# Kernel optimization log

Hardware: AMD Instinct MI355X
Metric: run time of the kernel (lower is better)

The kernel has to match this reference:

```python
import jax, jax.numpy as jnp
import numpy as np

N, E, B, D, L = 100000, 600000, 128, 128, 3
BOT = 64
EPS = 1e-5


def _forward(query_x, corpus_x, gin_eps, mlp_W1, mlp_b1, mlp_W2, mlp_b2, bn_gamma, bn_beta,
             pool_G1, pool_g1b, pool_G2, pool_g2b, pool_Wm,
             int_G1, int_g1b, int_G2, int_g2b, int_F1, int_f1b, int_F2, int_f2b,
             sc_G1, sc_g1b, sc_G2, sc_g2b, sc_F1, sc_f1b, sc_F2, sc_f2b,
             query_edge_index, query_graph_idx, corpus_edge_index, corpus_graph_idx, num_graphs):
    def gin(x, ei, l):
        # GINConv: sum of source-node features into targets, plus (1+eps)*self
        agg = jax.ops.segment_sum(x[ei[0]], ei[1], num_segments=x.shape[0])
        h = (1.0 + gin_eps[l]) * x + agg
        h = jax.nn.relu(h @ mlp_W1[l] + mlp_b1[l]) @ mlp_W2[l] + mlp_b2[l]
        mu = h.mean(axis=0)
        var = ((h - mu) ** 2).mean(axis=0)  # biased var (BatchNorm training mode)
        h = (h - mu) * jax.lax.rsqrt(var + EPS) * bn_gamma[l] + bn_beta[l]
        return jax.nn.relu(h)  # dropout p=0.0

    def pool(x, gidx, l):
        coef = jnp.tanh(jax.nn.relu(x @ pool_G1[l] + pool_g1b[l]) @ pool_G2[l] + pool_g2b[l])
        s = (coef + 1.0) * x
        sums = jax.ops.segment_sum(s, gidx, num_segments=num_graphs)
        cnt = jax.ops.segment_sum(jnp.ones((x.shape[0],), x.dtype), gidx, num_segments=num_graphs)
        mean = sums / cnt[:, None]
        gc = jnp.tanh(mean @ pool_Wm[l])  # [B, D]
        node_coef = jax.nn.sigmoid(jnp.sum(s * gc[gidx], axis=1))  # [N]
        return jax.ops.segment_sum(node_coef[:, None] * s, gidx, num_segments=num_graphs)

    def interact(q, c, l):
        comb = jnp.concatenate([q, c], axis=1)  # [B, 2D]
        coef = jax.nn.sigmoid(jax.nn.relu(comb @ int_G1[l] + int_g1b[l]) @ int_G2[l] + int_g2b[l])
        sc = (coef + 1.0) * comb
        return jax.nn.relu(jax.nn.relu(sc @ int_F1[l] + int_f1b[l]) @ int_F2[l] + int_f2b[l])

    qx, cx = query_x, corpus_x
    feats = []
    for l in range(gin_eps.shape[0]):
        qx = gin(qx, query_edge_index, l)
        cx = gin(cx, corpus_edge_index, l)
        feats.append(interact(pool(qx, query_graph_idx, l), pool(cx, corpus_graph_idx, l), l))
    f = jnp.concatenate(feats, axis=1)  # [B, sum(filters)//2]
    coef = jax.nn.sigmoid(jax.nn.relu(f @ sc_G1 + sc_g1b) @ sc_G2 + sc_g2b)
    sf = (coef + 1.0) * f
    return (jax.nn.relu(sf @ sc_F1 + sc_f1b) @ sc_F2 + sc_f2b).squeeze(-1)  # [B]


def setup_inputs() -> dict:
    key = jax.random.key(0)
    kit = iter(jax.random.split(key, 64))
    def nrm(shape, s=0.05):
        return jax.random.normal(next(kit), shape, jnp.float32) * s
    C, R, OUT, AGG, RG = 2 * D, (2 * D) // 4, D // 2, (3 * D) // 2, ((3 * D) // 2) // 4
    inp = {
        "query_x": nrm((N, D), 1.0),
        "query_edge_index": jax.random.randint(next(kit), (2, E), 0, N),
        "query_graph_idx": jnp.sort(jax.random.randint(next(kit), (N,), 0, B)),
        "corpus_x": nrm((N, D), 1.0),
        "corpus_edge_index": jax.random.randint(next(kit), (2, E), 0, N),
        "corpus_graph_idx": jnp.sort(jax.random.randint(next(kit), (N,), 0, B)),
        "num_graphs": B,
        "gin_eps": jnp.zeros((L,), jnp.float32),
        "mlp_W1": nrm((L, D, D)), "mlp_b1": jnp.zeros((L, D)),
        "mlp_W2": nrm((L, D, D)), "mlp_b2": jnp.zeros((L, D)),
        "bn_gamma": jnp.ones((L, D)), "bn_beta": jnp.zeros((L, D)),
        "pool_G1": nrm((L, D, D // 4)), "pool_g1b": jnp.zeros((L, D // 4)),
        "pool_G2": nrm((L, D // 4, D)), "pool_g2b": jnp.zeros((L, D)),
        "pool_Wm": nrm((L, D, D)),
        "int_G1": nrm((L, C, R)), "int_g1b": jnp.zeros((L, R)),
        "int_G2": nrm((L, R, C)), "int_g2b": jnp.zeros((L, C)),
        "int_F1": nrm((L, C, C)), "int_f1b": jnp.zeros((L, C)),
        "int_F2": nrm((L, C, OUT)), "int_f2b": jnp.zeros((L, OUT)),
        "sc_G1": nrm((AGG, RG)), "sc_g1b": jnp.zeros((RG,)),
        "sc_G2": nrm((RG, AGG)), "sc_g2b": jnp.zeros((AGG,)),
        "sc_F1": nrm((AGG, BOT)), "sc_f1b": jnp.zeros((BOT,)),
        "sc_F2": nrm((BOT, 1)), "sc_f2b": jnp.zeros((1,)),
    }
    return inp


def reference(query_x, query_edge_index, query_graph_idx, corpus_x, corpus_edge_index, corpus_graph_idx,
              num_graphs, gin_eps, mlp_W1, mlp_b1, mlp_W2, mlp_b2, bn_gamma, bn_beta,
              pool_G1, pool_g1b, pool_G2, pool_g2b, pool_Wm,
              int_G1, int_g1b, int_G2, int_g2b, int_F1, int_f1b, int_F2, int_f2b,
              sc_G1, sc_g1b, sc_G2, sc_g2b, sc_F1, sc_f1b, sc_F2, sc_f2b):
    return _forward(query_x, corpus_x, gin_eps, mlp_W1, mlp_b1, mlp_W2, mlp_b2, bn_gamma, bn_beta,
                    pool_G1, pool_g1b, pool_G2, pool_g2b, pool_Wm,
                    int_G1, int_g1b, int_G2, int_g2b, int_F1, int_f1b, int_F2, int_f2b,
                    sc_G1, sc_g1b, sc_G2, sc_g2b, sc_F1, sc_f1b, sc_F2, sc_f2b,
                    query_edge_index, query_graph_idx, corpus_edge_index, corpus_graph_idx, num_graphs)
```

## Files before the change

kernel.cpp:

```cpp
#include <hip/hip_runtime.h>
#include <hip/hip_bf16.h>

constexpr int NN  = 100000;
constexpr int NN2 = 200000;
constexpr int NE  = 600000;
constexpr int NB  = 128;
constexpr int D   = 128;
constexpr int NL  = 3;
constexpr int CAP = 48;
constexpr int MT_TOT = NN2 / 16;
constexpr int MT_Q   = NN / 16;

typedef __bf16 bf16x8 __attribute__((ext_vector_type(8)));
typedef float f32x4 __attribute__((ext_vector_type(4)));
typedef unsigned short us8 __attribute__((ext_vector_type(8)));

__device__ __forceinline__ float sigmoidf_(float x) { return 1.0f / (1.0f + __expf(-x)); }
__device__ __forceinline__ unsigned short f2b(float f) {
    __hip_bfloat16 h = __float2bfloat16(f);
    return __builtin_bit_cast(unsigned short, h);
}
__device__ __forceinline__ float b2f(unsigned short u) {
    __hip_bfloat16 h = __builtin_bit_cast(__hip_bfloat16, u);
    return __bfloat162float(h);
}
__device__ __forceinline__ bf16x8 ldfrag(const unsigned short* p) {
    return __builtin_bit_cast(bf16x8, *(const us8*)p);
}

__global__ __launch_bounds__(256) void k_csr_fill(const int* __restrict__ qei, const int* __restrict__ cei,
                                                  int* __restrict__ deg, int* __restrict__ bucket) {
    int e = blockIdx.x * 256 + threadIdx.x;
    int src, dst;
    if (e < NE) {
        src = qei[e]; dst = qei[NE + e];
    } else if (e < 2 * NE) {
        src = cei[e - NE] + NN; dst = cei[NE + (e - NE)] + NN;
    } else return;
    int pos = atomicAdd(&deg[dst], 1);
    if (pos < CAP) bucket[(size_t)dst * CAP + pos] = src;
}

__global__ __launch_bounds__(256) void k_cnt(const int* __restrict__ gq, const int* __restrict__ gc,
                                             float* __restrict__ cnt) {
    __shared__ float h[256];
    for (int i = threadIdx.x; i < 256; i += 256) h[i] = 0.f;
    __syncthreads();
    int total = gridDim.x * 256;
    int tid = blockIdx.x * 256 + threadIdx.x;
    int per = (NN2 + total - 1) / total;
    int r0 = tid * per, r1 = min(r0 + per, NN2);
    if (r0 < r1) {
        int cur = (r0 < NN) ? gq[r0] : 128 + gc[r0 - NN];
        float c = 0.f;
        for (int r = r0; r < r1; ++r) {
            int g = (r < NN) ? gq[r] : 128 + gc[r - NN];
            if (g != cur) { atomicAdd(&h[cur], c); c = 0.f; cur = g; }
            c += 1.f;
        }
        atomicAdd(&h[cur], c);
    }
    __syncthreads();
    for (int i = threadIdx.x; i < 256; i += 256)
        if (h[i] != 0.f) atomicAdd(&cnt[i], h[i]);
}

__global__ __launch_bounds__(256) void k_wprep_all(
    const float* mW1, const float* mW2, const float* pG1, const float* pG2,
    const float* iG1, const float* iG2, const float* iF1, const float* iF2,
    const float* sG1, const float* sG2, const float* sF1,
    unsigned short* W1t, unsigned short* W2t, unsigned short* G1t, unsigned short* G2t,
    unsigned short* iG1t, unsigned short* iG2t, unsigned short* iF1t, unsigned short* iF2t,
    unsigned short* sG1t, unsigned short* sG2t, unsigned short* sF1t) {
    int i = blockIdx.x * 256 + threadIdx.x;
#define SEG(CNT, KK, NN_, SRC, DST)                                              \
    if (i < (CNT)) {                                                             \
        int l = i / ((KK) * (NN_)), r = i % ((KK) * (NN_));                      \
        int n = r / (KK), k = r % (KK);                                          \
        DST[i] = f2b(SRC[(size_t)l * (KK) * (NN_) + (size_t)k * (NN_) + n]);     \
        return;                                                                  \
    }                                                                            \
    i -= (CNT);
    SEG(49152, 128, 128, mW1, W1t)
    SEG(49152, 128, 128, mW2, W2t)
    SEG(12288, 128, 32, pG1, G1t)
    SEG(12288, 32, 128, pG2, G2t)
    SEG(49152, 256, 64, iG1, iG1t)
    SEG(49152, 64, 256, iG2, iG2t)
    SEG(196608, 256, 256, iF1, iF1t)
    SEG(49152, 256, 64, iF2, iF2t)
    SEG(9216, 192, 48, sG1, sG1t)
    if (i < 12288) {
        int n = i / 64, k = i % 64;
        sG2t[i] = (k < 48) ? f2b(sG2[(size_t)k * 192 + n]) : (unsigned short)0;
        return;
    }
    i -= 12288;
    SEG(12288, 192, 64, sF1, sF1t)
#undef SEG
}

template <bool BF16IN>
__global__ __launch_bounds__(256) void k_gather(const float* __restrict__ qx, const float* __restrict__ cx,
                                                const unsigned short* __restrict__ xb, unsigned short* __restrict__ z,
                                                const int* __restrict__ deg, const int* __restrict__ bucket,
                                                const float* __restrict__ eps_p, int l) {
    int r = blockIdx.x * 16 + (threadIdx.x >> 4);
    int c8 = threadIdx.x & 15;
    float e = 1.0f + eps_p[l];
    float a[8];
    const float* base = nullptr; int off = 0;
    if constexpr (BF16IN) {
        us8 v = *(const us8*)(xb + (size_t)r * D + c8 * 8);
#pragma unroll
        for (int j = 0; j < 8; ++j) a[j] = e * b2f(v[j]);
    } else {
        base = (r < NN) ? qx : cx; off = (r < NN) ? 0 : NN;
        float4 v0 = *(const float4*)(base + (size_t)(r - off) * D + c8 * 8);
        float4 v1 = *(const float4*)(base + (size_t)(r - off) * D + c8 * 8 + 4);
        a[0] = e * v0.x; a[1] = e * v0.y; a[2] = e * v0.z; a[3] = e * v0.w;
        a[4] = e * v1.x; a[5] = e * v1.y; a[6] = e * v1.z; a[7] = e * v1.w;
    }
    int d = deg[r]; d = (d < CAP) ? d : CAP;
    const int* bk = bucket + (size_t)r * CAP;
    int i = 0;
    for (; i + 4 <= d; i += 4) {
        int s0 = bk[i], s1 = bk[i + 1], s2 = bk[i + 2], s3 = bk[i + 3];
        if constexpr (BF16IN) {
            us8 u0 = *(const us8*)(xb + (size_t)s0 * D + c8 * 8);
            us8 u1 = *(const us8*)(xb + (size_t)s1 * D + c8 * 8);
            us8 u2 = *(const us8*)(xb + (size_t)s2 * D + c8 * 8);
            us8 u3 = *(const us8*)(xb + (size_t)s3 * D + c8 * 8);
#pragma unroll
            for (int j = 0; j < 8; ++j)
                a[j] += b2f(u0[j]) + b2f(u1[j]) + b2f(u2[j]) + b2f(u3[j]);
        } else {
            const float* p0 = base + (size_t)(s0 - off) * D + c8 * 8;
            const float* p1 = base + (size_t)(s1 - off) * D + c8 * 8;
            const float* p2 = base + (size_t)(s2 - off) * D + c8 * 8;
            const float* p3 = base + (size_t)(s3 - off) * D + c8 * 8;
            float4 w0 = *(const float4*)p0, w0b = *(const float4*)(p0 + 4);
            float4 w1 = *(const float4*)p1, w1b = *(const float4*)(p1 + 4);
            float4 w2 = *(const float4*)p2, w2b = *(const float4*)(p2 + 4);
            float4 w3 = *(const float4*)p3, w3b = *(const float4*)(p3 + 4);
            a[0] += w0.x + w1.x + w2.x + w3.x; a[1] += w0.y + w1.y + w2.y + w3.y;
            a[2] += w0.z + w1.z + w2.z + w3.z; a[3] += w0.w + w1.w + w2.w + w3.w;
            a[4] += w0b.x + w1b.x + w2b.x + w3b.x; a[5] += w0b.y + w1b.y + w2b.y + w3b.y;
            a[6] += w0b.z + w1b.z + w2b.z + w3b.z; a[7] += w0b.w + w1b.w + w2b.w + w3b.w;
        }
    }
    for (; i < d; ++i) {
        int s0 = bk[i];
        if constexpr (BF16IN) {
            us8 u0 = *(const us8*)(xb + (size_t)s0 * D + c8 * 8);
#pragma unroll
            for (int j = 0; j < 8; ++j) a[j] += b2f(u0[j]);
        } else {
            const float* p0 = base + (size_t)(s0 - off) * D + c8 * 8;
            float4 w0 = *(const float4*)p0, w0b = *(const float4*)(p0 + 4);
            a[0] += w0.x; a[1] += w0.y; a[2] += w0.z; a[3] += w0.w;
            a[4] += w0b.x; a[5] += w0b.y; a[6] += w0b.z; a[7] += w0b.w;
        }
    }
    us8 o;
#pragma unroll
    for (int j = 0; j < 8; ++j) o[j] = f2b(a[j]);
    *(us8*)(z + (size_t)r * D + c8 * 8) = o;
}

constexpr int HSTR = 136;
__global__ __launch_bounds__(256, 2) void k_mlp(unsigned short* zh,
                                                const unsigned short* __restrict__ W1t,
                                                const unsigned short* __restrict__ W2t,
                                                const float* __restrict__ b1,
                                                const float* __restrict__ b2,
                                                float* __restrict__ stat) {
    __shared__ unsigned short hb[2][2][16 * HSTR];
    __shared__ float red[512];
    int wave = threadIdx.x >> 6, lane = threadIdx.x & 63;
    int col16 = lane & 15, quad = lane >> 4;
    int g = wave >> 1, half = wave & 1;
    bf16x8 bf1[4][4], bf2[4][4];
    float bb1[4], bb2[4];
#pragma unroll
    for (int t = 0; t < 4; ++t) {
        int c = half * 64 + t * 16 + col16;
        bb1[t] = b1[c]; bb2[t] = b2[c];
#pragma unroll
        for (int kc = 0; kc < 4; ++kc) {
            bf1[t][kc] = ldfrag(W1t + (size_t)c * D + kc * 32 + quad * 8);
            bf2[t][kc] = ldfrag(W2t + (size_t)c * D + kc * 32 + quad * 8);
        }
    }
    float cs[2][4] = {{0.f,0.f,0.f,0.f},{0.f,0.f,0.f,0.f}};
    float cq[2][4] = {{0.f,0.f,0.f,0.f},{0.f,0.f,0.f,0.f}};
    int groups = gridDim.x * 2;
    int iters = (MT_TOT + groups - 1) / groups;
    for (int n = 0; n < iters; ++n) {
        int mt = blockIdx.x * 2 + g + n * groups;
        bool act = (mt < MT_TOT);
        int pp = n & 1;
        unsigned short* hbuf = hb[pp][g];
        {
            const unsigned short* Ap = zh + ((size_t)(act ? mt : 0) * 16 + col16) * D + quad * 8;
            f32x4 acc[4];
#pragma unroll
            for (int t = 0; t < 4; ++t) acc[t] = (f32x4){0.f, 0.f, 0.f, 0.f};
#pragma unroll
            for (int kc = 0; kc < 4; ++kc) {
                bf16x8 af = ldfrag(Ap + kc * 32);
#pragma unroll
                for (int t = 0; t < 4; ++t)
                    acc[t] = __builtin_amdgcn_mfma_f32_16x16x32_bf16(af, bf1[t][kc], acc[t], 0, 0, 0);
            }
#pragma unroll
            for (int t = 0; t < 4; ++t) {
                int c = half * 64 + t * 16 + col16;
#pragma unroll
                for (int r = 0; r < 4; ++r)
                    hbuf[(quad * 4 + r) * HSTR + c] = f2b(fmaxf(acc[t][r] + bb1[t], 0.f));
            }
        }
        __syncthreads();
        {
            f32x4 acc[4];
#pragma unroll
            for (int t = 0; t < 4; ++t) acc[t] = (f32x4){0.f, 0.f, 0.f, 0.f};
#pragma unroll
            for (int kc = 0; kc < 4; ++kc) {
                bf16x8 af = ldfrag(&hbuf[col16 * HSTR + kc * 32 + quad * 8]);
#pragma unroll
                for (int t = 0; t < 4; ++t)
                    acc[t] = __builtin_amdgcn_mfma_f32_16x16x32_bf16(af, bf2[t][kc], acc[t], 0, 0, 0);
            }
            if (act) {
                int side = (mt < MT_Q) ? 0 : 1;
#pragma unroll
                for (int t = 0; t < 4; ++t) {
                    int c = half * 64 + t * 16 + col16;
#pragma unroll
                    for (int r = 0; r < 4; ++r) {
                        int m = mt * 16 + quad * 4 + r;
                        float v = acc[t][r] + bb2[t];
                        zh[(size_t)m * D + c] = f2b(v);
                        cs[side][t] += v; cq[side][t] += v * v;
                    }
                }
            }
        }
    }
    for (int i = threadIdx.x; i < 512; i += 256) red[i] = 0.f;
    __syncthreads();
#pragma unroll
    for (int t = 0; t < 4; ++t) {
        int c = half * 64 + t * 16 + col16;
#pragma unroll
        for (int side = 0; side < 2; ++side) {
            atomicAdd(&red[side * 256 + c], cs[side][t]);
            atomicAdd(&red[side * 256 + 128 + c], cq[side][t]);
        }
    }
    __syncthreads();
    for (int i = threadIdx.x; i < 512; i += 256) atomicAdd(&stat[i], red[i]);
}

__global__ __launch_bounds__(256, 2) void k_pool(const unsigned short* __restrict__ H,
                                                 const unsigned short* __restrict__ G1t,
                                                 const unsigned short* __restrict__ G2t,
                                                 const float* __restrict__ b1,
                                                 const float* __restrict__ b2,
                                                 const float* __restrict__ stat,
                                                 const float* __restrict__ gamma,
                                                 const float* __restrict__ beta,
                                                 const int* __restrict__ gq, const int* __restrict__ gcix,
                                                 unsigned short* __restrict__ Xo,
                                                 unsigned short* __restrict__ S,
                                                 float* __restrict__ seg_sum) {
    __shared__ float sc_s[256], sh_s[256];
    __shared__ unsigned short xt[4][16 * HSTR];
    __shared__ unsigned short t2t[4][16 * 40];
    {
        int t = threadIdx.x, side = t >> 7, c = t & 127;
        const float invN = 1.0f / (float)NN;
        float mu = stat[side * 256 + c] * invN;
        float var = fmaxf(stat[side * 256 + 128 + c] * invN - mu * mu, 0.f);
        float inv = rsqrtf(var + 1e-5f);
        float s = gamma[c] * inv;
        sc_s[t] = s;
        sh_s[t] = beta[c] - mu * s;
    }
    __syncthreads();
    int wave = threadIdx.x >> 6, lane = threadIdx.x & 63;
    int col16 = lane & 15, quad = lane >> 4;
    unsigned short* xtile = xt[wave];
    unsigned short* t2tile = t2t[wave];
    int nwaves = gridDim.x * 4;
    int per = (MT_TOT + nwaves - 1) / nwaves;
    int wid = blockIdx.x * 4 + wave;
    int mt0 = wid * per, mt1 = min(mt0 + per, MT_TOT);
    if (mt0 >= mt1) return;

    bf16x8 g1f[2][4], g2f[8];
    float bb1[2], bb2[8];
#pragma unroll
    for (int t = 0; t < 2; ++t) {
        int c = t * 16 + col16;
        bb1[t] = b1[c];
#pragma unroll
        for (int kc = 0; kc < 4; ++kc)
            g1f[t][kc] = ldfrag(G1t + (size_t)c * D + kc * 32 + quad * 8);
    }
#pragma unroll
    for (int t = 0; t < 8; ++t) {
        int c = t * 16 + col16;
        bb2[t] = b2[c];
        g2f[t] = ldfrag(G2t + (size_t)c * 32 + quad * 8);
    }
    float sacc[8] = {0.f, 0.f, 0.f, 0.f, 0.f, 0.f, 0.f, 0.f};
    int curg = -1;
    for (int mt = mt0; mt < mt1; ++mt) {
        int side = (mt < MT_Q) ? 0 : 1;
        const float* scp = sc_s + side * 128;
        const float* shp = sh_s + side * 128;
        const unsigned short* Hp = H + ((size_t)mt * 16 + col16) * D + quad * 8;
        unsigned short* Xp = Xo + ((size_t)mt * 16 + col16) * D + quad * 8;
        f32x4 acc1[2];
#pragma unroll
        for (int t = 0; t < 2; ++t) acc1[t] = (f32x4){0.f, 0.f, 0.f, 0.f};
#pragma unroll
        for (int kc = 0; kc < 4; ++kc) {
            us8 hv = *(const us8*)(Hp + kc * 32);
            int k0 = kc * 32 + quad * 8;
            float4 s0 = *(const float4*)&scp[k0], s1 = *(const float4*)&scp[k0 + 4];
            float4 h0 = *(const float4*)&shp[k0], h1 = *(const float4*)&shp[k0 + 4];
            us8 xv;
            xv[0] = f2b(fmaxf(b2f(hv[0]) * s0.x + h0.x, 0.f));
            xv[1] = f2b(fmaxf(b2f(hv[1]) * s0.y + h0.y, 0.f));
            xv[2] = f2b(fmaxf(b2f(hv[2]) * s0.z + h0.z, 0.f));
            xv[3] = f2b(fmaxf(b2f(hv[3]) * s0.w + h0.w, 0.f));
            xv[4] = f2b(fmaxf(b2f(hv[4]) * s1.x + h1.x, 0.f));
            xv[5] = f2b(fmaxf(b2f(hv[5]) * s1.y + h1.y, 0.f));
            xv[6] = f2b(fmaxf(b2f(hv[6]) * s1.z + h1.z, 0.f));
            xv[7] = f2b(fmaxf(b2f(hv[7]) * s1.w + h1.w, 0.f));
            *(us8*)(Xp + kc * 32) = xv;
            *(us8*)(xtile + col16 * HSTR + k0) = xv;
            bf16x8 af = __builtin_bit_cast(bf16x8, xv);
#pragma unroll
            for (int t = 0; t < 2; ++t)
                acc1[t] = __builtin_amdgcn_mfma_f32_16x16x32_bf16(af, g1f[t][kc], acc1[t], 0, 0, 0);
        }
#pragma unroll
        for (int t = 0; t < 2; ++t) {
            int c = t * 16 + col16;
#pragma unroll
            for (int r = 0; r < 4; ++r)
                t2tile[(quad * 4 + r) * 40 + c] = f2b(fmaxf(acc1[t][r] + bb1[t], 0.f));
        }
        bf16x8 af2 = ldfrag(t2tile + col16 * 40 + quad * 8);
        f32x4 acc2[8];
#pragma unroll
        for (int t = 0; t < 8; ++t) {
            acc2[t] = (f32x4){0.f, 0.f, 0.f, 0.f};
            acc2[t] = __builtin_amdgcn_mfma_f32_16x16x32_bf16(af2, g2f[t], acc2[t], 0, 0, 0);
        }
#pragma unroll
        for (int r = 0; r < 4; ++r) {
            int m = mt * 16 + quad * 4 + r;
            int g = (m < NN) ? gq[m] : 128 + gcix[m - NN];
            if (g != curg) {
                if (curg >= 0) {
#pragma unroll
                    for (int t = 0; t < 8; ++t) {
                        atomicAdd(&seg_sum[(size_t)curg * D + t * 16 + col16], sacc[t]);
                        sacc[t] = 0.f;
                    }
                }
                curg = g;
            }
#pragma unroll
            for (int t = 0; t < 8; ++t) {
                int c = t * 16 + col16;
                float v = (tanhf(acc2[t][r] + bb2[t]) + 1.f) * b2f(xtile[(quad * 4 + r) * HSTR + c]);
                S[(size_t)m * D + c] = f2b(v);
                sacc[t] += v;
            }
        }
    }
    if (curg >= 0) {
#pragma unroll
        for (int t = 0; t < 8; ++t)
            atomicAdd(&seg_sum[(size_t)curg * D + t * 16 + col16], sacc[t]);
    }
}

__global__ void k_gc(const float* __restrict__ sums, const float* __restrict__ cnt,
                     const float* __restrict__ Wm, float* __restrict__ gc) {
    __shared__ float m[D];
    int b = blockIdx.x, j = threadIdx.x;
    m[j] = sums[b * D + j] / cnt[b];
    __syncthreads();
    float a = 0.f;
#pragma unroll 8
    for (int i = 0; i < D; ++i) a += m[i] * Wm[i * D + j];
    gc[b * D + j] = tanhf(a);
}

__global__ __launch_bounds__(256) void k_ncseg(const unsigned short* __restrict__ S,
                                               const int* __restrict__ gq, const int* __restrict__ gc,
                                               const float* __restrict__ gcb,
                                               float* __restrict__ dq, float* __restrict__ dc) {
    int stream = blockIdx.x * 4 + (threadIdx.x >> 6);
    int lane = threadIdx.x & 63;
    int nstream = gridDim.x * 4;
    int per = (NN2 + nstream - 1) / nstream;
    int r0 = stream * per;
    int r1 = min(r0 + per, NN2);
    if (r0 >= r1) return;
    float a0 = 0.f, a1 = 0.f;
    int cur = (r0 < NN) ? gq[r0] : 128 + gc[r0 - NN];
    for (int r = r0; r < r1; ++r) {
        int g = (r < NN) ? gq[r] : 128 + gc[r - NN];
        if (g != cur) {
            float* base = (cur < 128) ? (dq + cur * D) : (dc + (cur - 128) * D);
            atomicAdd(&base[lane * 2], a0);
            atomicAdd(&base[lane * 2 + 1], a1);
            a0 = 0.f; a1 = 0.f; cur = g;
        }
        ushort2 sv = *(const ushort2*)&S[(size_t)r * D + lane * 2];
        float2 gv = *(const float2*)&gcb[(size_t)g * D + lane * 2];
        float v0 = b2f(sv.x), v1 = b2f(sv.y);
        float p = v0 * gv.x + v1 * gv.y;
#pragma unroll
        for (int off = 1; off < 64; off <<= 1) p += __shfl_xor(p, off, 64);
        float nc = sigmoidf_(p);
        a0 += nc * v0; a1 += nc * v1;
    }
    float* base = (cur < 128) ? (dq + cur * D) : (dc + (cur - 128) * D);
    atomicAdd(&base[lane * 2], a0);
    atomicAdd(&base[lane * 2 + 1], a1);
}

constexpr int LSTR = 264;
__global__ __launch_bounds__(256) void k_interact(const float* __restrict__ pooled,
                                                  const unsigned short* __restrict__ iG1t, const float* __restrict__ ig1b,
                                                  const unsigned short* __restrict__ iG2t, const float* __restrict__ ig2b,
                                                  const unsigned short* __restrict__ iF1t, const float* __restrict__ if1b,
                                                  const unsigned short* __restrict__ iF2t, const float* __restrict__ if2b,
                                                  unsigned short* __restrict__ featsb) {
    __shared__ unsigned short bufC[16 * LSTR];
    __shared__ unsigned short bufA[16 * LSTR];
    __shared__ unsigned short bufB[16 * LSTR];
    int t = threadIdx.x, wave = t >> 6, lane = t & 63;
    int col16 = lane & 15, quad = lane >> 4;
    int pg = blockIdx.x & 7, l = blockIdx.x >> 3;
    int p0 = pg * 16;
    {
        int r = t >> 4, c0 = (t & 15) * 16;
        const float* src = (c0 < 128)
            ? (pooled + (size_t)l * NB * D + (size_t)(p0 + r) * D + c0)
            : (pooled + (size_t)(NL + l) * NB * D + (size_t)(p0 + r) * D + (c0 - 128));
#pragma unroll
        for (int j = 0; j < 16; ++j) bufC[r * LSTR + c0 + j] = f2b(src[j]);
    }
    __syncthreads();
    {
        f32x4 acc = (f32x4){0.f, 0.f, 0.f, 0.f};
        int n = wave * 16 + col16;
#pragma unroll
        for (int kc = 0; kc < 8; ++kc) {
            bf16x8 af = ldfrag(&bufC[col16 * LSTR + kc * 32 + quad * 8]);
            bf16x8 bfr = ldfrag(iG1t + ((size_t)l * 64 + n) * 256 + kc * 32 + quad * 8);
            acc = __builtin_amdgcn_mfma_f32_16x16x32_bf16(af, bfr, acc, 0, 0, 0);
        }
        float bb = ig1b[(size_t)l * 64 + n];
#pragma unroll
        for (int r = 0; r < 4; ++r)
            bufA[(quad * 4 + r) * LSTR + n] = f2b(fmaxf(acc[r] + bb, 0.f));
    }
    __syncthreads();
    {
        f32x4 acc[4];
#pragma unroll
        for (int tt = 0; tt < 4; ++tt) acc[tt] = (f32x4){0.f, 0.f, 0.f, 0.f};
#pragma unroll
        for (int kc = 0; kc < 2; ++kc) {
            bf16x8 af = ldfrag(&bufA[col16 * LSTR + kc * 32 + quad * 8]);
#pragma unroll
            for (int tt = 0; tt < 4; ++tt) {
                int n = wave * 64 + tt * 16 + col16;
                bf16x8 bfr = ldfrag(iG2t + ((size_t)l * 256 + n) * 64 + kc * 32 + quad * 8);
                acc[tt] = __builtin_amdgcn_mfma_f32_16x16x32_bf16(af, bfr, acc[tt], 0, 0, 0);
            }
        }
#pragma unroll
        for (int tt = 0; tt < 4; ++tt) {
            int n = wave * 64 + tt * 16 + col16;
            float bb = ig2b[(size_t)l * 256 + n];
#pragma unroll
            for (int r = 0; r < 4; ++r) {
                int row = quad * 4 + r;
                float s = (sigmoidf_(acc[tt][r] + bb) + 1.f) * b2f(bufC[row * LSTR + n]);
                bufB[row * LSTR + n] = f2b(s);
            }
        }
    }
    __syncthreads();
    {
        f32x4 acc[4];
#pragma unroll
        for (int tt = 0; tt < 4; ++tt) acc[tt] = (f32x4){0.f, 0.f, 0.f, 0.f};
#pragma unroll
        for (int kc = 0; kc < 8; ++kc) {
            bf16x8 af = ldfrag(&bufB[col16 * LSTR + kc * 32 + quad * 8]);
#pragma unroll
            for (int tt = 0; tt < 4; ++tt) {
                int n = wave * 64 + tt * 16 + col16;
                bf16x8 bfr = ldfrag(iF1t + (size_t)l * 256 * 256 + (size_t)n * 256 + kc * 32 + quad * 8);
                acc[tt] = __builtin_amdgcn_mfma_f32_16x16x32_bf16(af, bfr, acc[tt], 0, 0, 0);
            }
        }
#pragma unroll
        for (int tt = 0; tt < 4; ++tt) {
            int n = wave * 64 + tt * 16 + col16;
            float bb = if1b[(size_t)l * 256 + n];
#pragma unroll
            for (int r = 0; r < 4; ++r)
                bufA[(quad * 4 + r) * LSTR + n] = f2b(fmaxf(acc[tt][r] + bb, 0.f));
        }
    }
    __syncthreads();
    {
        f32x4 acc = (f32x4){0.f, 0.f, 0.f, 0.f};
        int n = wave * 16 + col16;
#pragma unroll
        for (int kc = 0; kc < 8; ++kc) {
            bf16x8 af = ldfrag(&bufA[col16 * LSTR + kc * 32 + quad * 8]);
            bf16x8 bfr = ldfrag(iF2t + ((size_t)l * 64 + n) * 256 + kc * 32 + quad * 8);
            acc = __builtin_amdgcn_mfma_f32_16x16x32_bf16(af, bfr, acc, 0, 0, 0);
        }
        float bb = if2b[(size_t)l * 64 + n];
#pragma unroll
        for (int r = 0; r < 4; ++r)
            featsb[(size_t)(p0 + quad * 4 + r) * 192 + l * 64 + n] = f2b(fmaxf(acc[r] + bb, 0.f));
    }
}

__global__ __launch_bounds__(256) void k_score(const unsigned short* __restrict__ featsb,
                                               const unsigned short* __restrict__ sG1t, const float* __restrict__ sg1b,
                                               const unsigned short* __restrict__ sG2t, const float* __restrict__ sg2b,
                                               const unsigned short* __restrict__ sF1t, const float* __restrict__ sf1b,
                                               const float* __restrict__ sF2, const float* __restrict__ sf2b,
                                               float* __restrict__ out) {
    __shared__ unsigned short bufF[16 * 200];
    __shared__ unsigned short bufA[16 * LSTR];
    __shared__ unsigned short bufB[16 * LSTR];
    __shared__ float redf[16 * 65];
    int t = threadIdx.x, wave = t >> 6, lane = t & 63;
    int col16 = lane & 15, quad = lane >> 4;
    int p0 = blockIdx.x * 16;
    {
        int r = t >> 4, c0 = (t & 15) * 12;
#pragma unroll
        for (int j = 0; j < 12; ++j)
            bufF[r * 200 + c0 + j] = featsb[(size_t)(p0 + r) * 192 + c0 + j];
    }
    __syncthreads();
    if (wave < 3) {
        f32x4 acc = (f32x4){0.f, 0.f, 0.f, 0.f};
        int n = wave * 16 + col16;
#pragma unroll
        for (int kc = 0; kc < 6; ++kc) {
            bf16x8 af = ldfrag(&bufF[col16 * 200 + kc * 32 + quad * 8]);
            bf16x8 bfr = ldfrag(sG1t + (size_t)n * 192 + kc * 32 + quad * 8);
            acc = __builtin_amdgcn_mfma_f32_16x16x32_bf16(af, bfr, acc, 0, 0, 0);
        }
        float bb = sg1b[n];
#pragma unroll
        for (int r = 0; r < 4; ++r)
            bufA[(quad * 4 + r) * LSTR + n] = f2b(fmaxf(acc[r] + bb, 0.f));
    } else {
        int row = lane >> 2, c = 48 + (lane & 3) * 4;
#pragma unroll
        for (int j = 0; j < 4; ++j) bufA[row * LSTR + c + j] = 0;
    }
    __syncthreads();
    {
        f32x4 acc[3];
#pragma unroll
        for (int tt = 0; tt < 3; ++tt) acc[tt] = (f32x4){0.f, 0.f, 0.f, 0.f};
#pragma unroll
        for (int kc = 0; kc < 2; ++kc) {
            bf16x8 af = ldfrag(&bufA[col16 * LSTR + kc * 32 + quad * 8]);
#pragma unroll
            for (int tt = 0; tt < 3; ++tt) {
                int n = wave * 48 + tt * 16 + col16;
                bf16x8 bfr = ldfrag(sG2t + (size_t)n * 64 + kc * 32 + quad * 8);
                acc[tt] = __builtin_amdgcn_mfma_f32_16x16x32_bf16(af, bfr, acc[tt], 0, 0, 0);
            }
        }
#pragma unroll
        for (int tt = 0; tt < 3; ++tt) {
            int n = wave * 48 + tt * 16 + col16;
            float bb = sg2b[n];
#pragma unroll
            for (int r = 0; r < 4; ++r) {
                int row = quad * 4 + r;
                float s = (sigmoidf_(acc[tt][r] + bb) + 1.f) * b2f(bufF[row * 200 + n]);
                bufB[row * LSTR + n] = f2b(s);
            }
        }
    }
    __syncthreads();
    {
        f32x4 acc = (f32x4){0.f, 0.f, 0.f, 0.f};
        int n = wave * 16 + col16;
#pragma unroll
        for (int kc = 0; kc < 6; ++kc) {
            bf16x8 af = ldfrag(&bufB[col16 * LSTR + kc * 32 + quad * 8]);
            bf16x8 bfr = ldfrag(sF1t + (size_t)n * 192 + kc * 32 + quad * 8);
            acc = __builtin_amdgcn_mfma_f32_16x16x32_bf16(af, bfr, acc, 0, 0, 0);
        }
        float bb = sf1b[n], w2 = sF2[n];
#pragma unroll
        for (int r = 0; r < 4; ++r)
            redf[(quad * 4 + r) * 65 + n] = fmaxf(acc[r] + bb, 0.f) * w2;
    }
    __syncthreads();
    if (t < 16) {
        float s = 0.f;
#pragma unroll 8
        for (int i = 0; i < 64; ++i) s += redf[t * 65 + i];
        out[p0 + t] = s + sf2b[0];
    }
}

extern "C" void kernel_launch(void* const* d_in, const int* in_sizes, int n_in,
                              void* d_out, int out_size, void* d_ws, size_t ws_size,
                              hipStream_t stream) {
    const float* query_x   = (const float*)d_in[0];
    const int*   query_ei  = (const int*)d_in[1];
    const int*   query_gi  = (const int*)d_in[2];
    const float* corpus_x  = (const float*)d_in[3];
    const int*   corpus_ei = (const int*)d_in[4];
    const int*   corpus_gi = (const int*)d_in[5];
    const float* gin_eps   = (const float*)d_in[7];
    const float* mlp_W1    = (const float*)d_in[8];
    const float* mlp_b1    = (const float*)d_in[9];
    const float* mlp_W2    = (const float*)d_in[10];
    const float* mlp_b2    = (const float*)d_in[11];
    const float* bn_gamma  = (const float*)d_in[12];
    const float* bn_beta   = (const float*)d_in[13];
    const float* pool_G1   = (const float*)d_in[14];
    const float* pool_g1b  = (const float*)d_in[15];
    const float* pool_G2   = (const float*)d_in[16];
    const float* pool_g2b  = (const float*)d_in[17];
    const float* pool_Wm   = (const float*)d_in[18];
    const float* int_G1    = (const float*)d_in[19];
    const float* int_g1b   = (const float*)d_in[20];
    const float* int_G2    = (const float*)d_in[21];
    const float* int_g2b   = (const float*)d_in[22];
    const float* int_F1    = (const float*)d_in[23];
    const float* int_f1b   = (const float*)d_in[24];
    const float* int_F2    = (const float*)d_in[25];
    const float* int_f2b   = (const float*)d_in[26];
    const float* sc_G1     = (const float*)d_in[27];
    const float* sc_g1b    = (const float*)d_in[28];
    const float* sc_G2     = (const float*)d_in[29];
    const float* sc_g2b    = (const float*)d_in[30];
    const float* sc_F1     = (const float*)d_in[31];
    const float* sc_f1b    = (const float*)d_in[32];
    const float* sc_F2     = (const float*)d_in[33];
    const float* sc_f2b    = (const float*)d_in[34];
    float* out = (float*)d_out;

    unsigned short* Zb  = (unsigned short*)d_ws;
    unsigned short* Xb  = Zb + (size_t)NN2 * D;
    unsigned short* Sb  = Xb + (size_t)NN2 * D;
    unsigned short* featsb = Sb + (size_t)NN2 * D;
    unsigned short* W1t = featsb + 128 * 192;
    unsigned short* W2t = W1t + NL * D * D;
    unsigned short* G1t = W2t + NL * D * D;
    unsigned short* G2t = G1t + NL * 32 * D;
    unsigned short* iG1t = G2t + NL * D * 32;
    unsigned short* iG2t = iG1t + NL * 64 * 256;
    unsigned short* iF1t = iG2t + NL * 256 * 64;
    unsigned short* iF2t = iF1t + NL * 256 * 256;
    unsigned short* sG1t = iF2t + NL * 64 * 256;
    unsigned short* sG2t = sG1t + 48 * 192;
    unsigned short* sF1t = sG2t + 192 * 64;
    int* deg    = (int*)(sF1t + 64 * 192);
    int* bucket = deg + NN2;
    float* bn_stat  = (float*)(bucket + (size_t)NN2 * CAP);
    float* seg_sum  = bn_stat + NL * 512;
    float* seg_cnt  = seg_sum + 256 * D;
    float* gcb      = seg_cnt + 256;
    float* pooled   = gcb + 256 * D;

    k_wprep_all<<<1956, 256, 0, stream>>>(mlp_W1, mlp_W2, pool_G1, pool_G2,
                                          int_G1, int_G2, int_F1, int_F2,
                                          sc_G1, sc_G2, sc_F1,
                                          W1t, W2t, G1t, G2t, iG1t, iG2t, iF1t, iF2t,
                                          sG1t, sG2t, sF1t);

    hipMemsetAsync(deg, 0, NN2 * sizeof(int), stream);
    hipMemsetAsync(bn_stat, 0, NL * 512 * sizeof(float), stream);
    hipMemsetAsync(pooled, 0, 2 * NL * NB * D * sizeof(float), stream);
    hipMemsetAsync(seg_cnt, 0, 256 * sizeof(float), stream);
    k_csr_fill<<<(2 * NE + 255) / 256, 256, 0, stream>>>(query_ei, corpus_ei, deg, bucket);
    k_cnt<<<64, 256, 0, stream>>>(query_gi, corpus_gi, seg_cnt);

    for (int l = 0; l < NL; ++l) {
        if (l == 0)
            k_gather<false><<<NN2 / 16, 256, 0, stream>>>(query_x, corpus_x, nullptr, Zb,
                                                          deg, bucket, gin_eps, l);
        else
            k_gather<true><<<NN2 / 16, 256, 0, stream>>>(nullptr, nullptr, Xb, Zb,
                                                         deg, bucket, gin_eps, l);
        k_mlp<<<1024, 256, 0, stream>>>(Zb, W1t + (size_t)l * D * D, W2t + (size_t)l * D * D,
                                        mlp_b1 + l * D, mlp_b2 + l * D, bn_stat + l * 512);
        hipMemsetAsync(seg_sum, 0, 256 * D * sizeof(float), stream);
        k_pool<<<782, 256, 0, stream>>>(Zb, G1t + (size_t)l * 32 * D, G2t + (size_t)l * D * 32,
                                        pool_g1b + l * 32, pool_g2b + l * D,
                                        bn_stat + l * 512, bn_gamma + l * D, bn_beta + l * D,
                                        query_gi, corpus_gi, Xb, Sb, seg_sum);
        k_gc<<<256, D, 0, stream>>>(seg_sum, seg_cnt, pool_Wm + (size_t)l * D * D, gcb);
        k_ncseg<<<1024, 256, 0, stream>>>(Sb, query_gi, corpus_gi, gcb,
                                          pooled + (size_t)l * NB * D,
                                          pooled + (size_t)(NL + l) * NB * D);
    }
    k_interact<<<24, 256, 0, stream>>>(pooled, iG1t, int_g1b, iG2t, int_g2b,
                                       iF1t, int_f1b, iF2t, int_f2b, featsb);
    k_score<<<8, 256, 0, stream>>>(featsb, sG1t, sc_g1b, sG2t, sc_g2b,
                                   sF1t, sc_f1b, sc_F2, sc_f2b, out);
}
```

Measured before the change: 1.070 ms.

## Fuse node-coefficient pooling with next layer's gather and merge prep kernels

The per-layer node-coefficient segment reduction (ncseg) for layer l-1 now runs in the same launch as the neighbour gather for layer l, with block ranges split between the two jobs. Only the last layer keeps a standalone ncseg. The CSR fill, weight prep and count kernels are merged into one launch, and the per-layer seg_sum memset is replaced by zeroing inside k_gc after the values are read. The aim is fewer launches and memsets, and letting the latency-bound ncseg overlap with the bandwidth-bound gather. In exchange, the heterogeneous blocks in one grid may schedule unevenly, and correctness now depends on the buffer-reuse ordering across layers.

Measured after the change: 998.4 us. 1.07x faster.

```diff
diff --git a/kernel.cpp b/kernel.cpp
--- a/kernel.cpp
+++ b/kernel.cpp
@@ -11,6 +11,13 @@
 constexpr int MT_TOT = NN2 / 16;
 constexpr int MT_Q   = NN / 16;
 
+constexpr int PREP_CSR   = (2 * NE + 255) / 256;
+constexpr int PREP_WPREP = 1956;
+constexpr int PREP_CNT   = 64;
+constexpr int PREP_TOT   = PREP_CSR + PREP_WPREP + PREP_CNT;
+
+constexpr int NCSEG_BLK = 1024;
+
 typedef __bf16 bf16x8 __attribute__((ext_vector_type(8)));
 typedef float f32x4 __attribute__((ext_vector_type(4)));
 typedef unsigned short us8 __attribute__((ext_vector_type(8)));
@@ -28,144 +35,220 @@
     return __builtin_bit_cast(bf16x8, *(const us8*)p);
 }
 
-__global__ __launch_bounds__(256) void k_csr_fill(const int* __restrict__ qei, const int* __restrict__ cei,
-                                                  int* __restrict__ deg, int* __restrict__ bucket) {
-    int e = blockIdx.x * 256 + threadIdx.x;
-    int src, dst;
-    if (e < NE) {
-        src = qei[e]; dst = qei[NE + e];
-    } else if (e < 2 * NE) {
-        src = cei[e - NE] + NN; dst = cei[NE + (e - NE)] + NN;
-    } else return;
-    int pos = atomicAdd(&deg[dst], 1);
-    if (pos < CAP) bucket[(size_t)dst * CAP + pos] = src;
-}
-
-__global__ __launch_bounds__(256) void k_cnt(const int* __restrict__ gq, const int* __restrict__ gc,
-                                             float* __restrict__ cnt) {
-    __shared__ float h[256];
-    for (int i = threadIdx.x; i < 256; i += 256) h[i] = 0.f;
-    __syncthreads();
-    int total = gridDim.x * 256;
-    int tid = blockIdx.x * 256 + threadIdx.x;
-    int per = (NN2 + total - 1) / total;
-    int r0 = tid * per, r1 = min(r0 + per, NN2);
-    if (r0 < r1) {
-        int cur = (r0 < NN) ? gq[r0] : 128 + gc[r0 - NN];
-        float c = 0.f;
-        for (int r = r0; r < r1; ++r) {
-            int g = (r < NN) ? gq[r] : 128 + gc[r - NN];
-            if (g != cur) { atomicAdd(&h[cur], c); c = 0.f; cur = g; }
-            c += 1.f;
-        }
-        atomicAdd(&h[cur], c);
-    }
-    __syncthreads();
-    for (int i = threadIdx.x; i < 256; i += 256)
-        if (h[i] != 0.f) atomicAdd(&cnt[i], h[i]);
-}
-
-__global__ __launch_bounds__(256) void k_wprep_all(
+__device__ __forceinline__ void ncseg_body(int vbid, int nstream_blocks,
+                                           const unsigned short* __restrict__ S,
+                                           const int* __restrict__ gq, const int* __restrict__ gc,
+                                           const float* __restrict__ gcb,
+                                           float* __restrict__ dq, float* __restrict__ dc) {
+    int stream = vbid * 4 + (threadIdx.x >> 6);
+    int lane = threadIdx.x & 63;
+    int nstream = nstream_blocks * 4;
+    int per = (NN2 + nstream - 1) / nstream;
+    int r0 = stream * per;
+    int r1 = min(r0 + per, NN2);
+    if (r0 >= r1) return;
+    float a0 = 0.f, a1 = 0.f;
+    int cur = (r0 < NN) ? gq[r0] : 128 + gc[r0 - NN];
+    for (int r = r0; r < r1; ++r) {
+        int g = (r < NN) ? gq[r] : 128 + gc[r - NN];
+        if (g != cur) {
+            float* base = (cur < 128) ? (dq + cur * D) : (dc + (cur - 128) * D);
+            atomicAdd(&base[lane * 2], a0);
+            atomicAdd(&base[lane * 2 + 1], a1);
+            a0 = 0.f; a1 = 0.f; cur = g;
+        }
+        ushort2 sv = *(const ushort2*)&S[(size_t)r * D + lane * 2];
+        float2 gv = *(const float2*)&gcb[(size_t)g * D + lane * 2];
+        float v0 = b2f(sv.x), v1 = b2f(sv.y);
+        float p = v0 * gv.x + v1 * gv.y;
+#pragma unroll
+        for (int off = 1; off < 64; off <<= 1) p += __shfl_xor(p, off, 64);
+        float nc = sigmoidf_(p);
+        a0 += nc * v0; a1 += nc * v1;
+    }
+    float* base = (cur < 128) ? (dq + cur * D) : (dc + (cur - 128) * D);
+    atomicAdd(&base[lane * 2], a0);
+    atomicAdd(&base[lane * 2 + 1], a1);
+}
+
+__device__ __forceinline__ void gather_bf16_body(int vbid,
+                                                 const unsigned short* __restrict__ xb,
+                                                 unsigned short* __restrict__ z,
+                                                 const int* __restrict__ deg, const int* __restrict__ bucket,
+                                                 float e) {
+    int r = vbid * 16 + (threadIdx.x >> 4);
+    int c8 = threadIdx.x & 15;
+    float a[8];
+    us8 v = *(const us8*)(xb + (size_t)r * D + c8 * 8);
+#pragma unroll
+    for (int j = 0; j < 8; ++j) a[j] = e * b2f(v[j]);
+    int d = deg[r]; d = (d < CAP) ? d : CAP;
+    const int* bk = bucket + (size_t)r * CAP;
+    int i = 0;
+    for (; i + 4 <= d; i += 4) {
+        int s0 = bk[i], s1 = bk[i + 1], s2 = bk[i + 2], s3 = bk[i + 3];
+        us8 u0 = *(const us8*)(xb + (size_t)s0 * D + c8 * 8);
+        us8 u1 = *(const us8*)(xb + (size_t)s1 * D + c8 * 8);
+        us8 u2 = *(const us8*)(xb + (size_t)s2 * D + c8 * 8);
+        us8 u3 = *(const us8*)(xb + (size_t)s3 * D + c8 * 8);
+#pragma unroll
+        for (int j = 0; j < 8; ++j)
+            a[j] += b2f(u0[j]) + b2f(u1[j]) + b2f(u2[j]) + b2f(u3[j]);
+    }
+    for (; i < d; ++i) {
+        int s0 = bk[i];
+        us8 u0 = *(const us8*)(xb + (size_t)s0 * D + c8 * 8);
+#pragma unroll
+        for (int j = 0; j < 8; ++j) a[j] += b2f(u0[j]);
+    }
+    us8 o;
+#pragma unroll
+    for (int j = 0; j < 8; ++j) o[j] = f2b(a[j]);
+    *(us8*)(z + (size_t)r * D + c8 * 8) = o;
+}
+
+__global__ __launch_bounds__(256) void k_prep(
+    const int* __restrict__ qei, const int* __restrict__ cei,
+    int* __restrict__ deg, int* __restrict__ bucket,
     const float* mW1, const float* mW2, const float* pG1, const float* pG2,
     const float* iG1, const float* iG2, const float* iF1, const float* iF2,
     const float* sG1, const float* sG2, const float* sF1,
     unsigned short* W1t, unsigned short* W2t, unsigned short* G1t, unsigned short* G2t,
     unsigned short* iG1t, unsigned short* iG2t, unsigned short* iF1t, unsigned short* iF2t,
-    unsigned short* sG1t, unsigned short* sG2t, unsigned short* sF1t) {
-    int i = blockIdx.x * 256 + threadIdx.x;
+    unsigned short* sG1t, unsigned short* sG2t, unsigned short* sF1t,
+    const int* __restrict__ gq, const int* __restrict__ gc, float* __restrict__ cnt) {
+    if (blockIdx.x < PREP_CSR) {
+        int e = blockIdx.x * 256 + threadIdx.x;
+        int src, dst;
+        if (e < NE) {
+            src = qei[e]; dst = qei[NE + e];
+        } else if (e < 2 * NE) {
+            src = cei[e - NE] + NN; dst = cei[NE + (e - NE)] + NN;
+        } else return;
+        int pos = atomicAdd(&deg[dst], 1);
+        if (pos < CAP) bucket[(size_t)dst * CAP + pos] = src;
+        return;
+    }
+    if (blockIdx.x < PREP_CSR + PREP_WPREP) {
+        int i = (blockIdx.x - PREP_CSR) * 256 + threadIdx.x;
 #define SEG(CNT, KK, NN_, SRC, DST)                                              \
-    if (i < (CNT)) {                                                             \
-        int l = i / ((KK) * (NN_)), r = i % ((KK) * (NN_));                      \
-        int n = r / (KK), k = r % (KK);                                          \
-        DST[i] = f2b(SRC[(size_t)l * (KK) * (NN_) + (size_t)k * (NN_) + n]);     \
-        return;                                                                  \
-    }                                                                            \
-    i -= (CNT);
-    SEG(49152, 128, 128, mW1, W1t)
-    SEG(49152, 128, 128, mW2, W2t)
-    SEG(12288, 128, 32, pG1, G1t)
-    SEG(12288, 32, 128, pG2, G2t)
-    SEG(49152, 256, 64, iG1, iG1t)
-    SEG(49152, 64, 256, iG2, iG2t)
-    SEG(196608, 256, 256, iF1, iF1t)
-    SEG(49152, 256, 64, iF2, iF2t)
-    SEG(9216, 192, 48, sG1, sG1t)
-    if (i < 12288) {
-        int n = i / 64, k = i % 64;
-        sG2t[i] = (k < 48) ? f2b(sG2[(size_t)k * 192 + n]) : (unsigned short)0;
+        if (i < (CNT)) {                                                         \
+            int l = i / ((KK) * (NN_)), r = i % ((KK) * (NN_));                  \
+            int n = r / (KK), k = r % (KK);                                      \
+            DST[i] = f2b(SRC[(size_t)l * (KK) * (NN_) + (size_t)k * (NN_) + n]); \
+            return;                                                              \
+        }                                                                        \
+        i -= (CNT);
+        SEG(49152, 128, 128, mW1, W1t)
+        SEG(49152, 128, 128, mW2, W2t)
+        SEG(12288, 128, 32, pG1, G1t)
+        SEG(12288, 32, 128, pG2, G2t)
+        SEG(49152, 256, 64, iG1, iG1t)
+        SEG(49152, 64, 256, iG2, iG2t)
+        SEG(196608, 256, 256, iF1, iF1t)
+        SEG(49152, 256, 64, iF2, iF2t)
+        SEG(9216, 192, 48, sG1, sG1t)
+        if (i < 12288) {
+            int n = i / 64, k = i % 64;
+            sG2t[i] = (k < 48) ? f2b(sG2[(size_t)k * 192 + n]) : (unsigned short)0;
+            return;
+        }
+        i -= 12288;
+        SEG(12288, 192, 64, sF1, sF1t)
+#undef SEG
         return;
     }
-    i -= 12288;
-    SEG(12288, 192, 64, sF1, sF1t)
-#undef SEG
-}
-
-template <bool BF16IN>
-__global__ __launch_bounds__(256) void k_gather(const float* __restrict__ qx, const float* __restrict__ cx,
-                                                const unsigned short* __restrict__ xb, unsigned short* __restrict__ z,
-                                                const int* __restrict__ deg, const int* __restrict__ bucket,
-                                                const float* __restrict__ eps_p, int l) {
+    {
+        __shared__ float h[256];
+        int vb = blockIdx.x - (PREP_CSR + PREP_WPREP);
+        for (int i = threadIdx.x; i < 256; i += 256) h[i] = 0.f;
+        __syncthreads();
+        int total = PREP_CNT * 256;
+        int tid = vb * 256 + threadIdx.x;
+        int per = (NN2 + total - 1) / total;
+        int r0 = tid * per, r1 = min(r0 + per, NN2);
+        if (r0 < r1) {
+            int cur = (r0 < NN) ? gq[r0] : 128 + gc[r0 - NN];
+            float c = 0.f;
+            for (int r = r0; r < r1; ++r) {
+                int g = (r < NN) ? gq[r] : 128 + gc[r - NN];
+                if (g != cur) { atomicAdd(&h[cur], c); c = 0.f; cur = g; }
+                c += 1.f;
+            }
+            atomicAdd(&h[cur], c);
+        }
+        __syncthreads();
+        for (int i = threadIdx.x; i < 256; i += 256)
+            if (h[i] != 0.f) atomicAdd(&cnt[i], h[i]);
+    }
+}
+
+__global__ __launch_bounds__(256) void k_gather0(const float* __restrict__ qx, const float* __restrict__ cx,
+                                                 unsigned short* __restrict__ z,
+                                                 const int* __restrict__ deg, const int* __restrict__ bucket,
+                                                 const float* __restrict__ eps_p) {
     int r = blockIdx.x * 16 + (threadIdx.x >> 4);
     int c8 = threadIdx.x & 15;
-    float e = 1.0f + eps_p[l];
+    float e = 1.0f + eps_p[0];
     float a[8];
-    const float* base = nullptr; int off = 0;
-    if constexpr (BF16IN) {
-        us8 v = *(const us8*)(xb + (size_t)r * D + c8 * 8);
-#pragma unroll
-        for (int j = 0; j < 8; ++j) a[j] = e * b2f(v[j]);
-    } else {
-        base = (r < NN) ? qx : cx; off = (r < NN) ? 0 : NN;
-        float4 v0 = *(const float4*)(base + (size_t)(r - off) * D + c8 * 8);
-        float4 v1 = *(const float4*)(base + (size_t)(r - off) * D + c8 * 8 + 4);
-        a[0] = e * v0.x; a[1] = e * v0.y; a[2] = e * v0.z; a[3] = e * v0.w;
-        a[4] = e * v1.x; a[5] = e * v1.y; a[6] = e * v1.z; a[7] = e * v1.w;
-    }
+    const float* base = (r < NN) ? qx : cx;
+    int off = (r < NN) ? 0 : NN;
+    float4 v0 = *(const float4*)(base + (size_t)(r - off) * D + c8 * 8);
+    float4 v1 = *(const float4*)(base + (size_t)(r - off) * D + c8 * 8 + 4);
+    a[0] = e * v0.x; a[1] = e * v0.y; a[2] = e * v0.z; a[3] = e * v0.w;
+    a[4] = e * v1.x; a[5] = e * v1.y; a[6] = e * v1.z; a[7] = e * v1.w;
     int d = deg[r]; d = (d < CAP) ? d : CAP;
     const int* bk = bucket + (size_t)r * CAP;
     int i = 0;
     for (; i + 4 <= d; i += 4) {
         int s0 = bk[i], s1 = bk[i + 1], s2 = bk[i + 2], s3 = bk[i + 3];
-        if constexpr (BF16IN) {
-            us8 u0 = *(const us8*)(xb + (size_t)s0 * D + c8 * 8);
-            us8 u1 = *(const us8*)(xb + (size_t)s1 * D + c8 * 8);
-            us8 u2 = *(const us8*)(xb + (size_t)s2 * D + c8 * 8);
-            us8 u3 = *(const us8*)(xb + (size_t)s3 * D + c8 * 8);
-#pragma unroll
-            for (int j = 0; j < 8; ++j)
-                a[j] += b2f(u0[j]) + b2f(u1[j]) + b2f(u2[j]) + b2f(u3[j]);
-        } else {
-            const float* p0 = base + (size_t)(s0 - off) * D + c8 * 8;
-            const float* p1 = base + (size_t)(s1 - off) * D + c8 * 8;
-            const float* p2 = base + (size_t)(s2 - off) * D + c8 * 8;
-            const float* p3 = base + (size_t)(s3 - off) * D + c8 * 8;
-            float4 w0 = *(const float4*)p0, w0b = *(const float4*)(p0 + 4);
-            float4 w1 = *(const float4*)p1, w1b = *(const float4*)(p1 + 4);
-            float4 w2 = *(const float4*)p2, w2b = *(const float4*)(p2 + 4);
-            float4 w3 = *(const float4*)p3, w3b = *(const float4*)(p3 + 4);
-            a[0] += w0.x + w1.x + w2.x + w3.x; a[1] += w0.y + w1.y + w2.y + w3.y;
-            a[2] += w0.z + w1.z + w2.z + w3.z; a[3] += w0.w + w1.w + w2.w + w3.w;
-            a[4] += w0b.x + w1b.x + w2b.x + w3b.x; a[5] += w0b.y + w1b.y + w2b.y + w3b.y;
-            a[6] += w0b.z + w1b.z + w2b.z + w3b.z; a[7] += w0b.w + w1b.w + w2b.w + w3b.w;
-        }
+        const float* p0 = base + (size_t)(s0 - off) * D + c8 * 8;
+        const float* p1 = base + (size_t)(s1 - off) * D + c8 * 8;
+        const float* p2 = base + (size_t)(s2 - off) * D + c8 * 8;
+        const float* p3 = base + (size_t)(s3 - off) * D + c8 * 8;
+        float4 w0 = *(const float4*)p0, w0b = *(const float4*)(p0 + 4);
+        float4 w1 = *(const float4*)p1, w1b = *(const float4*)(p1 + 4);
+        float4 w2 = *(const float4*)p2, w2b = *(const float4*)(p2 + 4);
+        float4 w3 = *(const float4*)p3, w3b = *(const float4*)(p3 + 4);
+        a[0] += w0.x + w1.x + w2.x + w3.x; a[1] += w0.y + w1.y + w2.y + w3.y;
+        a[2] += w0.z + w1.z + w2.z + w3.z; a[3] += w0.w + w1.w + w2.w + w3.w;
+        a[4] += w0b.x + w1b.x + w2b.x + w3b.x; a[5] += w0b.y + w1b.y + w2b.y + w3b.y;
+        a[6] += w0b.z + w1b.z + w2b.z + w3b.z; a[7] += w0b.w + w1b.w + w2b.w + w3b.w;
     }
     for (; i < d; ++i) {
         int s0 = bk[i];
-        if constexpr (BF16IN) {
-            us8 u0 = *(const us8*)(xb + (size_t)s0 * D + c8 * 8);
-#pragma unroll
-            for (int j = 0; j < 8; ++j) a[j] += b2f(u0[j]);
-        } else {
-            const float* p0 = base + (size_t)(s0 - off) * D + c8 * 8;
-            float4 w0 = *(const float4*)p0, w0b = *(const float4*)(p0 + 4);
-            a[0] += w0.x; a[1] += w0.y; a[2] += w0.z; a[3] += w0.w;
-            a[4] += w0b.x; a[5] += w0b.y; a[6] += w0b.z; a[7] += w0b.w;
-        }
+        const float* p0 = base + (size_t)(s0 - off) * D + c8 * 8;
+        float4 w0 = *(const float4*)p0, w0b = *(const float4*)(p0 + 4);
+        a[0] += w0.x; a[1] += w0.y; a[2] += w0.z; a[3] += w0.w;
+        a[4] += w0b.x; a[5] += w0b.y; a[6] += w0b.z; a[7] += w0b.w;
     }
     us8 o;
 #pragma unroll
     for (int j = 0; j < 8; ++j) o[j] = f2b(a[j]);
     *(us8*)(z + (size_t)r * D + c8 * 8) = o;
+}
+
+__global__ __launch_bounds__(256) void k_gncseg(const unsigned short* __restrict__ xb,
+                                                unsigned short* __restrict__ z,
+                                                const int* __restrict__ deg, const int* __restrict__ bucket,
+                                                const float* __restrict__ eps_p, int l,
+                                                const unsigned short* __restrict__ S,
+                                                const int* __restrict__ gq, const int* __restrict__ gcix,
+                                                const float* __restrict__ gcb,
+                                                float* __restrict__ dq, float* __restrict__ dc) {
+    if (blockIdx.x < NCSEG_BLK) {
+        ncseg_body(blockIdx.x, NCSEG_BLK, S, gq, gcix, gcb, dq, dc);
+    } else {
+        float e = 1.0f + eps_p[l];
+        gather_bf16_body(blockIdx.x - NCSEG_BLK, xb, z, deg, bucket, e);
+    }
+}
+
+__global__ __launch_bounds__(256) void k_ncseg(const unsigned short* __restrict__ S,
+                                               const int* __restrict__ gq, const int* __restrict__ gc,
+                                               const float* __restrict__ gcb,
+                                               float* __restrict__ dq, float* __restrict__ dc) {
+    ncseg_body(blockIdx.x, NCSEG_BLK, S, gq, gc, gcb, dq, dc);
 }
 
 constexpr int HSTR = 136;
@@ -393,51 +476,17 @@
     }
 }
 
-__global__ void k_gc(const float* __restrict__ sums, const float* __restrict__ cnt,
+__global__ void k_gc(float* __restrict__ sums, const float* __restrict__ cnt,
                      const float* __restrict__ Wm, float* __restrict__ gc) {
     __shared__ float m[D];
     int b = blockIdx.x, j = threadIdx.x;
     m[j] = sums[b * D + j] / cnt[b];
+    sums[b * D + j] = 0.f;
     __syncthreads();
     float a = 0.f;
 #pragma unroll 8
     for (int i = 0; i < D; ++i) a += m[i] * Wm[i * D + j];
     gc[b * D + j] = tanhf(a);
-}
-
-__global__ __launch_bounds__(256) void k_ncseg(const unsigned short* __restrict__ S,
-                                               const int* __restrict__ gq, const int* __restrict__ gc,
-                                               const float* __restrict__ gcb,
-                                               float* __restrict__ dq, float* __restrict__ dc) {
-    int stream = blockIdx.x * 4 + (threadIdx.x >> 6);
-    int lane = threadIdx.x & 63;
-    int nstream = gridDim.x * 4;
-    int per = (NN2 + nstream - 1) / nstream;
-    int r0 = stream * per;
-    int r1 = min(r0 + per, NN2);
-    if (r0 >= r1) return;
-    float a0 = 0.f, a1 = 0.f;
-    int cur = (r0 < NN) ? gq[r0] : 128 + gc[r0 - NN];
-    for (int r = r0; r < r1; ++r) {
-        int g = (r < NN) ? gq[r] : 128 + gc[r - NN];
-        if (g != cur) {
-            float* base = (cur < 128) ? (dq + cur * D) : (dc + (cur - 128) * D);
-            atomicAdd(&base[lane * 2], a0);
-            atomicAdd(&base[lane * 2 + 1], a1);
-            a0 = 0.f; a1 = 0.f; cur = g;
-        }
-        ushort2 sv = *(const ushort2*)&S[(size_t)r * D + lane * 2];
-        float2 gv = *(const float2*)&gcb[(size_t)g * D + lane * 2];
-        float v0 = b2f(sv.x), v1 = b2f(sv.y);
-        float p = v0 * gv.x + v1 * gv.y;
-#pragma unroll
-        for (int off = 1; off < 64; off <<= 1) p += __shfl_xor(p, off, 64);
-        float nc = sigmoidf_(p);
-        a0 += nc * v0; a1 += nc * v1;
-    }
-    float* base = (cur < 128) ? (dq + cur * D) : (dc + (cur - 128) * D);
-    atomicAdd(&base[lane * 2], a0);
-    atomicAdd(&base[lane * 2 + 1], a1);
 }
 
 constexpr int LSTR = 264;
@@ -696,38 +745,40 @@
     float* gcb      = seg_cnt + 256;
     float* pooled   = gcb + 256 * D;
 
-    k_wprep_all<<<1956, 256, 0, stream>>>(mlp_W1, mlp_W2, pool_G1, pool_G2,
-                                          int_G1, int_G2, int_F1, int_F2,
-                                          sc_G1, sc_G2, sc_F1,
-                                          W1t, W2t, G1t, G2t, iG1t, iG2t, iF1t, iF2t,
-                                          sG1t, sG2t, sF1t);
-
     hipMemsetAsync(deg, 0, NN2 * sizeof(int), stream);
     hipMemsetAsync(bn_stat, 0, NL * 512 * sizeof(float), stream);
     hipMemsetAsync(pooled, 0, 2 * NL * NB * D * sizeof(float), stream);
     hipMemsetAsync(seg_cnt, 0, 256 * sizeof(float), stream);
-    k_csr_fill<<<(2 * NE + 255) / 256, 256, 0, stream>>>(query_ei, corpus_ei, deg, bucket);
-    k_cnt<<<64, 256, 0, stream>>>(query_gi, corpus_gi, seg_cnt);
+    hipMemsetAsync(seg_sum, 0, 256 * D * sizeof(float), stream);
+
+    k_prep<<<PREP_TOT, 256, 0, stream>>>(query_ei, corpus_ei, deg, bucket,
+                                         mlp_W1, mlp_W2, pool_G1, pool_G2,
+                                         int_G1, int_G2, int_F1, int_F2,
+                                         sc_G1, sc_G2, sc_F1,
+                                         W1t, W2t, G1t, G2t, iG1t, iG2t, iF1t, iF2t,
+                                         sG1t, sG2t, sF1t,
+                                         query_gi, corpus_gi, seg_cnt);
 
     for (int l = 0; l < NL; ++l) {
         if (l == 0)
-            k_gather<false><<<NN2 / 16, 256, 0, stream>>>(query_x, corpus_x, nullptr, Zb,
-                                                          deg, bucket, gin_eps, l);
+            k_gather0<<<MT_TOT, 256, 0, stream>>>(query_x, corpus_x, Zb, deg, bucket, gin_eps);
         else
-            k_gather<true><<<NN2 / 16, 256, 0, stream>>>(nullptr, nullptr, Xb, Zb,
-                                                         deg, bucket, gin_eps, l);
+            k_gncseg<<<NCSEG_BLK + MT_TOT, 256, 0, stream>>>(
+                Xb, Zb, deg, bucket, gin_eps, l,
+                Sb, query_gi, corpus_gi, gcb,
+                pooled + (size_t)(l - 1) * NB * D,
+                pooled + (size_t)(NL + l - 1) * NB * D);
         k_mlp<<<1024, 256, 0, stream>>>(Zb, W1t + (size_t)l * D * D, W2t + (size_t)l * D * D,
                                         mlp_b1 + l * D, mlp_b2 + l * D, bn_stat + l * 512);
-        hipMemsetAsync(seg_sum, 0, 256 * D * sizeof(float), stream);
         k_pool<<<782, 256, 0, stream>>>(Zb, G1t + (size_t)l * 32 * D, G2t + (size_t)l * D * 32,
                                         pool_g1b + l * 32, pool_g2b + l * D,
                                         bn_stat + l * 512, bn_gamma + l * D, bn_beta + l * D,
                                         query_gi, corpus_gi, Xb, Sb, seg_sum);
         k_gc<<<256, D, 0, stream>>>(seg_sum, seg_cnt, pool_Wm + (size_t)l * D * D, gcb);
-        k_ncseg<<<1024, 256, 0, stream>>>(Sb, query_gi, corpus_gi, gcb,
-                                          pooled + (size_t)l * NB * D,
-                                          pooled + (size_t)(NL + l) * NB * D);
-    }
+    }
+    k_ncseg<<<NCSEG_BLK, 256, 0, stream>>>(Sb, query_gi, corpus_gi, gcb,
+                                           pooled + (size_t)(NL - 1) * NB * D,
+                                           pooled + (size_t)(2 * NL - 1) * NB * D);
     k_interact<<<24, 256, 0, stream>>>(pooled, iG1t, int_g1b, iG2t, int_g2b,
                                        iF1t, int_f1b, iF2t, int_f2b, featsb);
     k_score<<<8, 256, 0, stream>>>(featsb, sG1t, sc_g1b, sG2t, sc_g2b,
```
